# Kernel optimization log

Measured on AMD Instinct MI355X. Metric: run time of the kernel, lower is better.

The kernel has to match this reference:

```python
import jax, jax.numpy as jnp
import numpy as np

N, D, H, E, K = 16384, 1024, 4096, 8, 2
PROJ = min(D // 2, 256)  # 256
CLAMP_MAX = float(np.log(1.0 / 0.01))  # log(100)


def setup_inputs() -> dict:
    key = jax.random.key(0)
    ks = jax.random.split(key, 10)
    x = jax.random.normal(ks[0], (N, D), dtype=jnp.float32)
    # cosine gate params
    Wp = jax.random.normal(ks[1], (D, PROJ), dtype=jnp.float32) * (1.0 / np.sqrt(D))
    bp = jnp.zeros((PROJ,), dtype=jnp.float32)
    sim = jax.random.normal(ks[2], (PROJ, E), dtype=jnp.float32) * 0.01
    temp = jnp.full((1,), float(np.log(1.0 / 0.5)), dtype=jnp.float32)  # log(1/init_t)
    # expert FFN params (mmcv FFN: linear->GELU->linear, add_identity)
    W1 = jax.random.normal(ks[3], (E, D, H), dtype=jnp.float32) * (1.0 / np.sqrt(D))
    b1 = jnp.zeros((E, H), dtype=jnp.float32)
    W2 = jax.random.normal(ks[4], (E, H, D), dtype=jnp.float32) * (1.0 / np.sqrt(H))
    b2 = jnp.zeros((E, D), dtype=jnp.float32)
    return {"x": x, "Wp": Wp, "bp": bp, "sim": sim, "temp": temp,
            "W1": W1, "b1": b1, "W2": W2, "b2": b2}


def _l2norm(v, axis):
    # F.normalize: v / max(||v||, 1e-12)
    n = jnp.sqrt(jnp.sum(v * v, axis=axis, keepdims=True))
    return v / jnp.maximum(n, 1e-12)


def _gates(x, Wp, bp, sim, temp):
    proj = _l2norm(x @ Wp + bp, axis=1)          # [N, PROJ], row-normalized
    logits = proj @ _l2norm(sim, axis=0)          # [N, E] cosine similarities
    scale = jnp.exp(jnp.minimum(temp, CLAMP_MAX))
    logits = logits * scale
    top_v, top_i = jax.lax.top_k(logits, K)       # [N, K]
    top_g = jax.nn.softmax(top_v, axis=-1)        # softmax over top-k logits
    gates = jnp.zeros((x.shape[0], E), dtype=logits.dtype)
    gates = gates.at[jnp.arange(x.shape[0])[:, None], top_i].set(top_g)
    return gates


def reference(x, Wp, bp, sim, temp, W1, b1, W2, b2):
    gates = _gates(x, Wp, bp, sim, temp)          # [N, E], sparse (k nonzeros/row)
    # dispatch + per-expert FFN (add_identity) + gate-weighted combine.
    # gate==0 for non-selected experts, so masked dense accumulation matches
    # the sort/split/index_add combine exactly.
    out = jnp.zeros_like(x)
    for e in range(E):
        g = gates[:, e:e + 1]                      # [N, 1]
        h = jax.nn.gelu(x @ W1[e] + b1[e], approximate=False)
        f = h @ W2[e] + b2[e]
        out = out + g * (x + f)                    # FFN residual, gate multiply
    return out
```

## Files before the change

kernel.cpp:

```cpp
#include <hip/hip_runtime.h>
#include <hip/hip_bf16.h>
#include <math.h>

#define N_TOK 16384
#define DIM   1024
#define HID   4096
#define NEXP  8
#define NPROJ 256
#define CLAMP_MAXD 4.605170185988091
#define CLAMP_MAXF 4.605170185988091f
#define TAUB 2e-3f

#define MAX_TILES 264
#define MAX_ROWS (MAX_TILES*128)
#define CHUNK_TILES 66
#define NCHUNK 4
#define CHUNK_ROWS (CHUNK_TILES*128)

#define M_CNT   0
#define M_CUR   8
#define M_ROWST 16
#define M_TILEST 25
#define M_TOT   34
#define M_RED   35

typedef __bf16 bf16x8 __attribute__((ext_vector_type(8)));
typedef float  floatx4 __attribute__((ext_vector_type(4)));

__device__ __forceinline__ unsigned short f2bfbits(float f) {
  __hip_bfloat16 b = __float2bfloat16(f);
  union { __hip_bfloat16 b; unsigned short u; } c; c.b = b; return c.u;
}
__device__ __forceinline__ float bf2f(unsigned short u) {
  union { unsigned int u; float f; } c; c.u = ((unsigned int)u) << 16; return c.f;
}
__device__ __forceinline__ float gelu_exact(float z) {
  return 0.5f * z * (1.0f + erff(z * 0.70710678118654752f));
}

__device__ __forceinline__ void gld16(void* lds, const void* g) {
  __builtin_amdgcn_global_load_lds(
      (const __attribute__((address_space(1))) void*)g,
      (__attribute__((address_space(3))) void*)lds, 16, 0, 0);
}


__global__ void k_zero_meta(int* meta) { meta[threadIdx.x] = 0; }

__global__ __launch_bounds__(256) void k_simn(const float* __restrict__ sim,
                                              double* __restrict__ simn,
                                              float* __restrict__ simnf) {
  __shared__ double norms[NEXP];
  int t = threadIdx.x;
  if (t < NEXP) {
    double s = 0.0;
    for (int j = 0; j < NPROJ; ++j) { double v = (double)sim[j*NEXP + t]; s += v*v; }
    double n = sqrt(s); norms[t] = (n > 1e-12 ? n : 1e-12);
  }
  __syncthreads();
  for (int q = 0; q < (NPROJ*NEXP)/256; ++q) {
    int idx = t + q*256; int e = idx & (NEXP-1);
    double v = (double)sim[idx] / norms[e];
    simn[idx] = v; simnf[idx] = (float)v;
  }
}

__global__ __launch_bounds__(256) void k_transpose(const float* __restrict__ in,
                                                   unsigned short* __restrict__ out,
                                                   int R, int C) {
  __shared__ float tile[32][33];
  size_t zoff = (size_t)blockIdx.z * (size_t)R * (size_t)C;
  in += zoff; out += zoff;
  int c  = blockIdx.x*32 + threadIdx.x;
  int r0 = blockIdx.y*32 + threadIdx.y;
  #pragma unroll
  for (int i = 0; i < 4; ++i)
    tile[threadIdx.y + i*8][threadIdx.x] = in[(size_t)(r0 + i*8)*C + c];
  __syncthreads();
  int r  = blockIdx.y*32 + threadIdx.x;
  int c0 = blockIdx.x*32 + threadIdx.y;
  #pragma unroll
  for (int i = 0; i < 4; ++i)
    out[(size_t)(c0 + i*8)*R + r] = f2bfbits(tile[threadIdx.x][threadIdx.y + i*8]);
}

__global__ __launch_bounds__(256) void k_tobf16(const float* __restrict__ x,
                                                unsigned short* __restrict__ xbf) {
  const float4* src = (const float4*)x;
  ushort4* dst = (ushort4*)xbf;
  const int n4 = N_TOK*DIM/4;
  for (int i = blockIdx.x*256 + threadIdx.x; i < n4; i += gridDim.x*256) {
    float4 v = src[i];
    ushort4 o; o.x=f2bfbits(v.x); o.y=f2bfbits(v.y); o.z=f2bfbits(v.z); o.w=f2bfbits(v.w);
    dst[i] = o;
  }
}

__global__ __launch_bounds__(256) void k_gate(const float* __restrict__ proj,
    const float* __restrict__ simnf, const float* __restrict__ temp,
    float* __restrict__ gates, int* __restrict__ eidx, int* __restrict__ meta,
    int* __restrict__ redoList) {
  __shared__ float sn[NPROJ*NEXP];
  __shared__ int hist[NEXP];
  int tid = threadIdx.x;
  if (tid < NEXP) hist[tid] = 0;
  #pragma unroll
  for (int q = 0; q < NPROJ*NEXP/256; ++q)
    sn[tid + q*256] = simnf[tid + q*256];
  __syncthreads();
  int token = blockIdx.x * 128 + (tid >> 1);
  int h = tid & 1;
  const float4* pr = (const float4*)(proj + (size_t)token*NPROJ + h*128);
  float s2 = 0.f;
  float lg[8];
  #pragma unroll
  for (int e = 0; e < 8; ++e) lg[e] = 0.f;
  #pragma unroll 4
  for (int j4 = 0; j4 < 32; ++j4) {
    float4 p4 = pr[j4];
    #pragma unroll
    for (int c = 0; c < 4; ++c) {
      float p = ((const float*)&p4)[c];
      s2 += p*p;
      const float* srow = &sn[(h*128 + j4*4 + c)*NEXP];
      float4 sa = *(const float4*)srow;
      float4 sb = *(const float4*)(srow + 4);
      lg[0] += p*sa.x; lg[1] += p*sa.y; lg[2] += p*sa.z; lg[3] += p*sa.w;
      lg[4] += p*sb.x; lg[5] += p*sb.y; lg[6] += p*sb.z; lg[7] += p*sb.w;
    }
  }
  s2 += __shfl_xor(s2, 1, 64);
  #pragma unroll
  for (int e = 0; e < 8; ++e) lg[e] += __shfl_xor(lg[e], 1, 64);
  if (h == 0) {
    float den = sqrtf(s2); den = fmaxf(den, 1e-12f);
    float l[8];
    #pragma unroll
    for (int e = 0; e < 8; ++e) l[e] = lg[e] / den;
    int iA = 0; float vA = l[0];
    #pragma unroll
    for (int e = 1; e < 8; ++e) if (l[e] > vA) { vA = l[e]; iA = e; }
    int iB = -1; float vB = -1e30f;
    #pragma unroll
    for (int e = 0; e < 8; ++e) if (e != iA && l[e] > vB) { vB = l[e]; iB = e; }
    float vC = -1e30f;
    #pragma unroll
    for (int e = 0; e < 8; ++e) if (e != iA && e != iB && l[e] > vC) vC = l[e];
    if (vB - vC < TAUB) {
      int p = atomicAdd(&meta[M_RED], 1);
      redoList[p] = token;
    } else {
      float esc = expf(fminf(temp[0], CLAMP_MAXF));
      float ex = expf((vB - vA) * esc);
      float g0 = 1.f / (1.f + ex);
      gates[2*token] = g0; gates[2*token+1] = ex / (1.f + ex);
      eidx[2*token] = iA; eidx[2*token+1] = iB;
      atomicAdd(&hist[iA], 1); atomicAdd(&hist[iB], 1);
    }
  }
  __syncthreads();
  if (tid < NEXP && hist[tid] > 0) atomicAdd(&meta[M_CNT + tid], hist[tid]);
}

__global__ __launch_bounds__(256) void k_gredo(const float* __restrict__ x,
    const float* __restrict__ Wp, const float* __restrict__ bp,
    const double* __restrict__ simn, const float* __restrict__ temp,
    float* __restrict__ gates, int* __restrict__ eidx, int* __restrict__ meta,
    const int* __restrict__ redoList) {
  __shared__ double wred[4][9];
  int nredo = meta[M_RED];
  int tid = threadIdx.x, lane = tid & 63, wv = tid >> 6;
  for (int r = blockIdx.x; r < nredo; r += gridDim.x) {
    int i = redoList[r];
    const float* xr = x + (size_t)i*DIM;
    int j = tid;
    double acc = 0.0;
    for (int d = 0; d < DIM; d += 4) {
      float4 xv = *(const float4*)&xr[d];
      acc += (double)xv.x * (double)Wp[(size_t)(d+0)*NPROJ + j];
      acc += (double)xv.y * (double)Wp[(size_t)(d+1)*NPROJ + j];
      acc += (double)xv.z * (double)Wp[(size_t)(d+2)*NPROJ + j];
      acc += (double)xv.w * (double)Wp[(size_t)(d+3)*NPROJ + j];
    }
    double v = acc + (double)bp[j];
    double vals[9];
    vals[0] = v*v;
    #pragma unroll
    for (int e = 0; e < NEXP; ++e) vals[1+e] = v * simn[j*NEXP + e];
    #pragma unroll
    for (int off = 32; off > 0; off >>= 1)
      #pragma unroll
      for (int k = 0; k < 9; ++k) vals[k] += __shfl_xor(vals[k], off, 64);
    if (lane == 0)
      #pragma unroll
      for (int k = 0; k < 9; ++k) wred[wv][k] = vals[k];
    __syncthreads();
    if (tid == 0) {
      double s[9];
      #pragma unroll
      for (int k = 0; k < 9; ++k)
        s[k] = wred[0][k] + wred[1][k] + wred[2][k] + wred[3][k];
      double den = sqrt(s[0]); if (den < 1e-12) den = 1e-12;
      double tp = (double)temp[0]; if (tp > CLAMP_MAXD) tp = CLAMP_MAXD;
      double sc = exp(tp) / den;
      double l[NEXP];
      #pragma unroll
      for (int e = 0; e < NEXP; ++e) l[e] = s[e+1]*sc;
      int iA = 0; double vA = l[0];
      for (int e = 1; e < NEXP; ++e) if (l[e] > vA) { vA = l[e]; iA = e; }
      int iB = -1; double vB = -1e300;
      for (int e = 0; e < NEXP; ++e) if (e != iA && l[e] > vB) { vB = l[e]; iB = e; }
      double ex = exp(vB - vA);
      double g0 = 1.0/(1.0+ex);
      gates[2*i] = (float)g0; gates[2*i+1] = (float)(ex/(1.0+ex));
      eidx[2*i] = iA; eidx[2*i+1] = iB;
      atomicAdd(&meta[M_CNT + iA], 1); atomicAdd(&meta[M_CNT + iB], 1);
    }
    __syncthreads();
  }
}

__global__ void k_offsets(int* meta) {
  int accT = 0;
  for (int e = 0; e < NEXP; ++e) {
    meta[M_TILEST + e] = accT;
    meta[M_ROWST + e]  = accT * 128;
    accT += (meta[M_CNT + e] + 127) >> 7;
  }
  meta[M_TILEST + NEXP] = accT;
  meta[M_ROWST + NEXP]  = accT * 128;
  meta[M_TOT] = accT;
}

__global__ void k_inittok(int* tok) { tok[blockIdx.x*256 + threadIdx.x] = 0; }

__global__ void k_fill(const int* __restrict__ eidx, int* meta,
                       int* __restrict__ tok, int* __restrict__ rowOf) {
  int i = blockIdx.x*256 + threadIdx.x;
  if (i >= N_TOK) return;
  #pragma unroll
  for (int k = 0; k < 2; ++k) {
    int e = eidx[2*i + k];
    int pos = atomicAdd(&meta[M_CUR + e], 1);
    int row = meta[M_ROWST + e] + pos;
    tok[row] = i;
    rowOf[2*i + k] = row;
  }
}

union LdsU {
  struct { short A[2][128*64]; short B[2][128*64]; } s;
  float C[32*132];
};

template<int ACT>
__global__ __launch_bounds__(256) void k_gemm(
    const unsigned short* __restrict__ Abase, const int* __restrict__ rowmap, int aRowOff,
    const unsigned short* __restrict__ Bbase, long bExpStride,
    const float* __restrict__ biasBase, int biasStride,
    unsigned short* __restrict__ Cbase, int ldc, int cRowOff,
    const int* __restrict__ meta, int tileBase, int K, int nty) {
  __shared__ LdsU lds;
  int flat = (int)(blockIdx.y * gridDim.x + blockIdx.x);
  int nwg  = (int)(gridDim.x * gridDim.y);
  int q8 = nwg >> 3, r8 = nwg & 7;
  int xcd = flat & 7, sub = flat >> 3;
  int W = (xcd < r8 ? xcd * (q8 + 1) : r8 * (q8 + 1) + (xcd - r8) * q8) + sub;
  int bx = W / nty;
  int by = W - bx * nty;
  int rt = tileBase + by;
  int e = 0;
  if (ACT != 2) {
    if (rt >= meta[M_TOT]) return;
    #pragma unroll
    for (int q = 1; q < NEXP; ++q) if (rt >= meta[M_TILEST + q]) e = q;
  }
  const unsigned short* Bexp = Bbase + (size_t)e * (size_t)bExpStride;
  int tid = threadIdx.x;
  int lane = tid & 63, wv = tid >> 6, mw = wv >> 1, nw = wv & 1;
  int ntBase = bx * 128;
  int lr = lane >> 3;
  int sg = lane & 7;
  const unsigned short* aG[4]; const unsigned short* bG[4];
  #pragma unroll
  for (int jj = 0; jj < 4; ++jj) {
    int r = wv*32 + jj*8 + lr;
    int g = sg ^ (r & 7);
    int grow = rt*128 + r;
    int arow = rowmap ? rowmap[grow] : (grow - aRowOff);
    aG[jj] = Abase + (size_t)arow * (size_t)K + g*8;
    bG[jj] = Bexp + (size_t)(ntBase + r) * (size_t)K + g*8;
  }
  floatx4 acc[4][4];
  #pragma unroll
  for (int mi = 0; mi < 4; ++mi)
    #pragma unroll
    for (int ni = 0; ni < 4; ++ni) acc[mi][ni] = (floatx4){0.f,0.f,0.f,0.f};
  const int nK = K >> 6;
  #pragma unroll
  for (int jj = 0; jj < 4; ++jj) {
    gld16(&lds.s.A[0][(wv*32 + jj*8)*64], aG[jj]);
    gld16(&lds.s.B[0][(wv*32 + jj*8)*64], bG[jj]);
  }
  for (int kt = 0; kt < nK; ++kt) {
    int cur = kt & 1;
    if (kt + 1 < nK) {
      int nxt = cur ^ 1;
      #pragma unroll
      for (int jj = 0; jj < 4; ++jj) {
        gld16(&lds.s.A[nxt][(wv*32 + jj*8)*64], aG[jj] + ((kt + 1) << 6));
        gld16(&lds.s.B[nxt][(wv*32 + jj*8)*64], bG[jj] + ((kt + 1) << 6));
      }
      asm volatile("s_waitcnt vmcnt(8)" ::: "memory");
    } else {
      asm volatile("s_waitcnt vmcnt(0)" ::: "memory");
    }
    __builtin_amdgcn_s_barrier();
    const short* As = lds.s.A[cur];
    const short* Bs = lds.s.B[cur];
    #pragma unroll
    for (int ks = 0; ks < 2; ++ks) {
      int gk = ks*4 + (lane >> 4);
      bf16x8 af[4], bfr[4];
      #pragma unroll
      for (int mi = 0; mi < 4; ++mi) {
        int m = mw*64 + mi*16 + (lane & 15);
        af[mi] = *(const bf16x8*)&As[m*64 + (gk ^ (m & 7))*8];
      }
      #pragma unroll
      for (int ni = 0; ni < 4; ++ni) {
        int n = nw*64 + ni*16 + (lane & 15);
        bfr[ni] = *(const bf16x8*)&Bs[n*64 + (gk ^ (n & 7))*8];
      }
      #pragma unroll
      for (int mi = 0; mi < 4; ++mi)
        #pragma unroll
        for (int ni = 0; ni < 4; ++ni)
          acc[mi][ni] = __builtin_amdgcn_mfma_f32_16x16x32_bf16(af[mi], bfr[ni], acc[mi][ni], 0,0,0);
    }
    __builtin_amdgcn_s_barrier();
  }
  const float* bias = biasBase + (size_t)e * (size_t)biasStride + ntBase;
  #pragma unroll
  for (int p = 0; p < 4; ++p) {
    __syncthreads();
    int lrow0 = mw*16 + ((lane>>4)<<2);
    int lcol  = nw*64 + (lane & 15);
    #pragma unroll
    for (int ni = 0; ni < 4; ++ni)
      #pragma unroll
      for (int jj = 0; jj < 4; ++jj)
        lds.C[(lrow0 + jj)*132 + lcol + ni*16] = acc[p][ni][jj];
    __syncthreads();
    #pragma unroll
    for (int q = 0; q < 2; ++q) {
      int lin = tid + q*256;
      int r = lin >> 4, c8 = lin & 15;
      float4 v0 = *(float4*)&lds.C[r*132 + c8*8];
      float4 v1 = *(float4*)&lds.C[r*132 + c8*8 + 4];
      float4 b0 = ((const float4*)bias)[c8*2];
      float4 b1 = ((const float4*)bias)[c8*2 + 1];
      v0.x += b0.x; v0.y += b0.y; v0.z += b0.z; v0.w += b0.w;
      v1.x += b1.x; v1.y += b1.y; v1.z += b1.z; v1.w += b1.w;
      if (ACT == 1) {
        v0.x = gelu_exact(v0.x); v0.y = gelu_exact(v0.y);
        v0.z = gelu_exact(v0.z); v0.w = gelu_exact(v0.w);
        v1.x = gelu_exact(v1.x); v1.y = gelu_exact(v1.y);
        v1.z = gelu_exact(v1.z); v1.w = gelu_exact(v1.w);
      }
      int gm = rt*128 + (r>>4)*64 + p*16 + (r & 15) - cRowOff;
      if (ACT == 2) {
        float* Cf = (float*)Cbase;
        *(float4*)&Cf[(size_t)gm*(size_t)ldc + ntBase + c8*8] = v0;
        *(float4*)&Cf[(size_t)gm*(size_t)ldc + ntBase + c8*8 + 4] = v1;
      } else {
        union { unsigned short u[8]; int4 v; } o;
        o.u[0]=f2bfbits(v0.x); o.u[1]=f2bfbits(v0.y); o.u[2]=f2bfbits(v0.z); o.u[3]=f2bfbits(v0.w);
        o.u[4]=f2bfbits(v1.x); o.u[5]=f2bfbits(v1.y); o.u[6]=f2bfbits(v1.z); o.u[7]=f2bfbits(v1.w);
        *(int4*)&Cbase[(size_t)gm*(size_t)ldc + ntBase + c8*8] = o.v;
      }
    }
  }
}

__global__ __launch_bounds__(256) void k_combine(const float* __restrict__ x,
    const unsigned short* __restrict__ f, const int* __restrict__ rowOf,
    const float* __restrict__ gates, float* __restrict__ out) {
  int i = blockIdx.x, t = threadIdx.x;
  int r0 = rowOf[2*i], r1 = rowOf[2*i+1];
  float g0 = gates[2*i], g1 = gates[2*i+1];
  float4 xv = ((const float4*)(x + (size_t)i*DIM))[t];
  ushort4 a = ((const ushort4*)(f + (size_t)r0*DIM))[t];
  ushort4 b = ((const ushort4*)(f + (size_t)r1*DIM))[t];
  float4 o;
  o.x = xv.x + g0*bf2f(a.x) + g1*bf2f(b.x);
  o.y = xv.y + g0*bf2f(a.y) + g1*bf2f(b.y);
  o.z = xv.z + g0*bf2f(a.z) + g1*bf2f(b.z);
  o.w = xv.w + g0*bf2f(a.w) + g1*bf2f(b.w);
  ((float4*)(out + (size_t)i*DIM))[t] = o;
}

extern "C" void kernel_launch(void* const* d_in, const int* in_sizes, int n_in,
                              void* d_out, int out_size, void* d_ws, size_t ws_size,
                              hipStream_t stream) {
  const float* x    = (const float*)d_in[0];
  const float* Wp   = (const float*)d_in[1];
  const float* bp   = (const float*)d_in[2];
  const float* sim  = (const float*)d_in[3];
  const float* temp = (const float*)d_in[4];
  const float* W1   = (const float*)d_in[5];
  const float* b1   = (const float*)d_in[6];
  const float* W2   = (const float*)d_in[7];
  const float* b2   = (const float*)d_in[8];
  float* out = (float*)d_out;

  char* w = (char*)d_ws;
  auto carve = [&](size_t bytes) { char* p = w; w += (bytes + 255) & ~(size_t)255; return p; };
  int*            meta = (int*)           carve(64*sizeof(int));
  float*          gates= (float*)         carve((size_t)N_TOK*2*4);
  int*            eidx = (int*)           carve((size_t)N_TOK*2*4);
  int*            rowOf= (int*)           carve((size_t)N_TOK*2*4);
  int*            tok  = (int*)           carve((size_t)MAX_ROWS*4);
  int*            redoL= (int*)           carve((size_t)N_TOK*4);
  double*         simn = (double*)        carve((size_t)NPROJ*NEXP*8);
  float*          simnf= (float*)         carve((size_t)NPROJ*NEXP*4);
  unsigned short* xbf  = (unsigned short*)carve((size_t)N_TOK*DIM*2);
  unsigned short* W1t  = (unsigned short*)carve((size_t)NEXP*HID*DIM*2);
  unsigned short* W2t  = (unsigned short*)carve((size_t)NEXP*DIM*HID*2);
  unsigned short* h    = (unsigned short*)carve((size_t)CHUNK_ROWS*HID*2);
  unsigned short* f    = (unsigned short*)carve((size_t)MAX_ROWS*DIM*2);
  float*          proj = (float*)h;
  unsigned short* WpT  = (unsigned short*)(h + (size_t)N_TOK*NPROJ*2);

  hipLaunchKernelGGL(k_zero_meta, dim3(1), dim3(64), 0, stream, meta);
  hipLaunchKernelGGL(k_simn, dim3(1), dim3(256), 0, stream, sim, simn, simnf);
  hipLaunchKernelGGL(k_transpose, dim3(HID/32, DIM/32, NEXP), dim3(32,8), 0, stream, W1, W1t, DIM, HID);
  hipLaunchKernelGGL(k_transpose, dim3(DIM/32, HID/32, NEXP), dim3(32,8), 0, stream, W2, W2t, HID, DIM);
  hipLaunchKernelGGL(k_transpose, dim3(NPROJ/32, DIM/32, 1), dim3(32,8), 0, stream, Wp, WpT, DIM, NPROJ);
  hipLaunchKernelGGL(k_tobf16, dim3(2048), dim3(256), 0, stream, x, xbf);
  hipLaunchKernelGGL((k_gemm<2>), dim3(NPROJ/128, N_TOK/128), dim3(256), 0, stream,
      xbf, (const int*)nullptr, 0, WpT, 0L, bp, 0,
      (unsigned short*)proj, NPROJ, 0, meta, 0, DIM, N_TOK/128);
  hipLaunchKernelGGL(k_gate, dim3(N_TOK/128), dim3(256), 0, stream,
                     proj, simnf, temp, gates, eidx, meta, redoL);
  hipLaunchKernelGGL(k_gredo, dim3(128), dim3(256), 0, stream,
                     x, Wp, bp, simn, temp, gates, eidx, meta, redoL);
  hipLaunchKernelGGL(k_offsets, dim3(1), dim3(1), 0, stream, meta);
  hipLaunchKernelGGL(k_inittok, dim3(MAX_ROWS/256), dim3(256), 0, stream, tok);
  hipLaunchKernelGGL(k_fill, dim3(N_TOK/256), dim3(256), 0, stream, eidx, meta, tok, rowOf);
  for (int c = 0; c < NCHUNK; ++c) {
    hipLaunchKernelGGL((k_gemm<1>), dim3(HID/128, CHUNK_TILES), dim3(256), 0, stream,
        xbf, tok, 0, W1t, (long)HID*DIM, b1, HID,
        h, HID, c*CHUNK_ROWS, meta, c*CHUNK_TILES, DIM, CHUNK_TILES);
    hipLaunchKernelGGL((k_gemm<0>), dim3(DIM/128, CHUNK_TILES), dim3(256), 0, stream,
        h, (const int*)nullptr, c*CHUNK_ROWS, W2t, (long)DIM*HID, b2, DIM,
        f, DIM, 0, meta, c*CHUNK_TILES, HID, CHUNK_TILES);
  }
  hipLaunchKernelGGL(k_combine, dim3(N_TOK), dim3(256), 0, stream, x, f, rowOf, gates, out);
}
```

Baseline: 1.858 ms.

## Add fp32 intermediate gate-recheck stage before fp64 fallback

Tokens whose bf16 gate top-2 margin is ambiguous are first recomputed in fp32, four tokens per block so each Wp load is reused, with a tighter threshold. Only tokens still ambiguous go to a second list handled by the fp64 path, which now uses four independent accumulators to break the dependency chain. The aim is to cut the cost of the slow double-precision projection by running it on far fewer tokens. The trade-offs are an extra kernel launch and reliance on the fp32 threshold being safe enough to keep top-k selection exact.

```diff
diff --git a/kernel.cpp b/kernel.cpp
--- a/kernel.cpp
+++ b/kernel.cpp
@@ -10,6 +10,7 @@
 #define CLAMP_MAXD 4.605170185988091
 #define CLAMP_MAXF 4.605170185988091f
 #define TAUB 2e-3f
+#define TAU32 3e-4f
 
 #define MAX_TILES 264
 #define MAX_ROWS (MAX_TILES*128)
@@ -23,6 +24,7 @@
 #define M_TILEST 25
 #define M_TOT   34
 #define M_RED   35
+#define M_RED2  36
 
 typedef __bf16 bf16x8 __attribute__((ext_vector_type(8)));
 typedef float  floatx4 __attribute__((ext_vector_type(4)));
@@ -162,27 +164,120 @@
   if (tid < NEXP && hist[tid] > 0) atomicAdd(&meta[M_CNT + tid], hist[tid]);
 }
 
-__global__ __launch_bounds__(256) void k_gredo(const float* __restrict__ x,
+__global__ __launch_bounds__(256) void k_gredo32(const float* __restrict__ x,
+    const float* __restrict__ Wp, const float* __restrict__ bp,
+    const float* __restrict__ simnf, const float* __restrict__ temp,
+    float* __restrict__ gates, int* __restrict__ eidx, int* __restrict__ meta,
+    const int* __restrict__ redoList, int* __restrict__ redoList2) {
+  __shared__ float wred[4][4][9];
+  int nredo = meta[M_RED];
+  int tid = threadIdx.x, lane = tid & 63, wv = tid >> 6;
+  int j = tid;
+  for (int g = blockIdx.x; g*4 < nredo; g += gridDim.x) {
+    int cnt = nredo - g*4; if (cnt > 4) cnt = 4;
+    const float* xr[4];
+    int tok[4];
+    #pragma unroll
+    for (int t = 0; t < 4; ++t) {
+      int idx = g*4 + t; if (idx > nredo-1) idx = nredo-1;
+      tok[t] = redoList[idx];
+      xr[t] = x + (size_t)tok[t]*DIM;
+    }
+    float acc[4][4];
+    #pragma unroll
+    for (int t = 0; t < 4; ++t)
+      #pragma unroll
+      for (int q = 0; q < 4; ++q) acc[t][q] = 0.f;
+    for (int d = 0; d < DIM; d += 4) {
+      float4 xv[4];
+      #pragma unroll
+      for (int t = 0; t < 4; ++t) xv[t] = *(const float4*)&xr[t][d];
+      #pragma unroll
+      for (int dd = 0; dd < 4; ++dd) {
+        float wpv = Wp[(size_t)(d+dd)*NPROJ + j];
+        #pragma unroll
+        for (int t = 0; t < 4; ++t)
+          acc[t][dd] += ((const float*)&xv[t])[dd] * wpv;
+      }
+    }
+    float snv[8];
+    #pragma unroll
+    for (int e = 0; e < 8; ++e) snv[e] = simnf[j*NEXP + e];
+    float bpj = bp[j];
+    #pragma unroll
+    for (int t = 0; t < 4; ++t) {
+      float v = acc[t][0] + acc[t][1] + acc[t][2] + acc[t][3] + bpj;
+      float vals[9];
+      vals[0] = v*v;
+      #pragma unroll
+      for (int e = 0; e < 8; ++e) vals[1+e] = v * snv[e];
+      #pragma unroll
+      for (int off = 32; off > 0; off >>= 1)
+        #pragma unroll
+        for (int k = 0; k < 9; ++k) vals[k] += __shfl_xor(vals[k], off, 64);
+      if (lane == 0)
+        #pragma unroll
+        for (int k = 0; k < 9; ++k) wred[wv][t][k] = vals[k];
+    }
+    __syncthreads();
+    if (tid == 0) {
+      for (int t = 0; t < cnt; ++t) {
+        int i = tok[t];
+        float s[9];
+        #pragma unroll
+        for (int k = 0; k < 9; ++k)
+          s[k] = wred[0][t][k] + wred[1][t][k] + wred[2][t][k] + wred[3][t][k];
+        float den = sqrtf(s[0]); den = fmaxf(den, 1e-12f);
+        float l[8];
+        #pragma unroll
+        for (int e = 0; e < 8; ++e) l[e] = s[1+e] / den;
+        int iA = 0; float vA = l[0];
+        #pragma unroll
+        for (int e = 1; e < 8; ++e) if (l[e] > vA) { vA = l[e]; iA = e; }
+        int iB = -1; float vB = -1e30f;
+        #pragma unroll
+        for (int e = 0; e < 8; ++e) if (e != iA && l[e] > vB) { vB = l[e]; iB = e; }
+        float vC = -1e30f;
+        #pragma unroll
+        for (int e = 0; e < 8; ++e) if (e != iA && e != iB && l[e] > vC) vC = l[e];
+        if (vB - vC < TAU32) {
+          int p = atomicAdd(&meta[M_RED2], 1);
+          redoList2[p] = i;
+        } else {
+          float esc = expf(fminf(temp[0], CLAMP_MAXF));
+          float ex = expf((vB - vA) * esc);
+          float g0 = 1.f / (1.f + ex);
+          gates[2*i] = g0; gates[2*i+1] = ex / (1.f + ex);
+          eidx[2*i] = iA; eidx[2*i+1] = iB;
+          atomicAdd(&meta[M_CNT + iA], 1); atomicAdd(&meta[M_CNT + iB], 1);
+        }
+      }
+    }
+    __syncthreads();
+  }
+}
+
+__global__ __launch_bounds__(256) void k_gredo64(const float* __restrict__ x,
     const float* __restrict__ Wp, const float* __restrict__ bp,
     const double* __restrict__ simn, const float* __restrict__ temp,
     float* __restrict__ gates, int* __restrict__ eidx, int* __restrict__ meta,
-    const int* __restrict__ redoList) {
+    const int* __restrict__ redoList2) {
   __shared__ double wred[4][9];
-  int nredo = meta[M_RED];
+  int nredo = meta[M_RED2];
   int tid = threadIdx.x, lane = tid & 63, wv = tid >> 6;
   for (int r = blockIdx.x; r < nredo; r += gridDim.x) {
-    int i = redoList[r];
+    int i = redoList2[r];
     const float* xr = x + (size_t)i*DIM;
     int j = tid;
-    double acc = 0.0;
+    double a0 = 0.0, a1 = 0.0, a2 = 0.0, a3 = 0.0;
     for (int d = 0; d < DIM; d += 4) {
       float4 xv = *(const float4*)&xr[d];
-      acc += (double)xv.x * (double)Wp[(size_t)(d+0)*NPROJ + j];
-      acc += (double)xv.y * (double)Wp[(size_t)(d+1)*NPROJ + j];
-      acc += (double)xv.z * (double)Wp[(size_t)(d+2)*NPROJ + j];
-      acc += (double)xv.w * (double)Wp[(size_t)(d+3)*NPROJ + j];
-    }
-    double v = acc + (double)bp[j];
+      a0 += (double)xv.x * (double)Wp[(size_t)(d+0)*NPROJ + j];
+      a1 += (double)xv.y * (double)Wp[(size_t)(d+1)*NPROJ + j];
+      a2 += (double)xv.z * (double)Wp[(size_t)(d+2)*NPROJ + j];
+      a3 += (double)xv.w * (double)Wp[(size_t)(d+3)*NPROJ + j];
+    }
+    double v = (a0 + a1) + (a2 + a3) + (double)bp[j];
     double vals[9];
     vals[0] = v*v;
     #pragma unroll
@@ -422,6 +517,7 @@
   int*            rowOf= (int*)           carve((size_t)N_TOK*2*4);
   int*            tok  = (int*)           carve((size_t)MAX_ROWS*4);
   int*            redoL= (int*)           carve((size_t)N_TOK*4);
+  int*            redoL2=(int*)           carve((size_t)N_TOK*4);
   double*         simn = (double*)        carve((size_t)NPROJ*NEXP*8);
   float*          simnf= (float*)         carve((size_t)NPROJ*NEXP*4);
   unsigned short* xbf  = (unsigned short*)carve((size_t)N_TOK*DIM*2);
@@ -443,8 +539,10 @@
       (unsigned short*)proj, NPROJ, 0, meta, 0, DIM, N_TOK/128);
   hipLaunchKernelGGL(k_gate, dim3(N_TOK/128), dim3(256), 0, stream,
                      proj, simnf, temp, gates, eidx, meta, redoL);
-  hipLaunchKernelGGL(k_gredo, dim3(128), dim3(256), 0, stream,
-                     x, Wp, bp, simn, temp, gates, eidx, meta, redoL);
+  hipLaunchKernelGGL(k_gredo32, dim3(256), dim3(256), 0, stream,
+                     x, Wp, bp, simnf, temp, gates, eidx, meta, redoL, redoL2);
+  hipLaunchKernelGGL(k_gredo64, dim3(64), dim3(256), 0, stream,
+                     x, Wp, bp, simn, temp, gates, eidx, meta, redoL2);
   hipLaunchKernelGGL(k_offsets, dim3(1), dim3(1), 0, stream, meta);
   hipLaunchKernelGGL(k_inittok, dim3(MAX_ROWS/256), dim3(256), 0, stream, tok);
   hipLaunchKernelGGL(k_fill, dim3(N_TOK/256), dim3(256), 0, stream, eidx, meta, tok, rowOf);
```

Result: faster. 1.782 ms (-4.1%).
